# Kernel tuning notes

Measured on AMD Instinct MI355X. Metric: run time of the kernel, lower is better.

The kernel has to match this reference:

```python
import jax, jax.numpy as jnp
import numpy as np

MASK_SUB = 1000000.0  # the module subtracts 1e6 from masked scores (not -inf)

def setup_inputs() -> dict:
    key = jax.random.key(0)
    kq, kk, kv = jax.random.split(key, 3)
    B, S, D = 16, 2048, 64
    q = jax.random.normal(kq, (B, S, D), dtype=jnp.float32)
    k = jax.random.normal(kk, (B, S, D), dtype=jnp.float32)
    v = jax.random.normal(kv, (B, S, D), dtype=jnp.float32)
    return {"q": q, "k": k, "v": v}

def reference(q, k, v):
    d_k = k.shape[-1]
    s = k.shape[-2]
    # scores: [b, s_q, s_k]
    scores = jnp.einsum('bqd,bkd->bqk', q, k) / jnp.sqrt(jnp.asarray(d_k, q.dtype))
    # causal mask: strictly-upper-triangular entries get 1e6 subtracted (matches torch.triu diagonal=1)
    causal = jnp.triu(jnp.ones((s, s), dtype=bool), k=1)
    scores = jnp.where(causal[None, :, :], scores - MASK_SUB, scores)
    weights = jax.nn.softmax(scores, axis=-1)
    return jnp.einsum('bqk,bkd->bqd', weights, v)
```

## Files before the change

### kernel.cpp

```cpp
#include <hip/hip_runtime.h>
#include <stdint.h>


typedef __bf16 bf16x8 __attribute__((ext_vector_type(8)));
typedef float f32x4 __attribute__((ext_vector_type(4)));
typedef float f32x16 __attribute__((ext_vector_type(16)));
typedef uint32_t u32x4 __attribute__((ext_vector_type(4)));

#define NB 16
#define SL 2048
#define DH 64

__device__ __forceinline__ __bf16 f2bf(float f) {
    uint32_t u = __builtin_bit_cast(uint32_t, f);
    u += 0x7FFFu + ((u >> 16) & 1u);
    uint16_t h = (uint16_t)(u >> 16);
    return __builtin_bit_cast(__bf16, h);
}

__device__ __forceinline__ float bf2f(uint16_t u) {
    return __builtin_bit_cast(float, (uint32_t)u << 16);
}

__device__ __forceinline__ uint32_t cvtpk(float lo, float hi) {
    uint32_t r;
    asm("v_cvt_pk_bf16_f32 %0, %1, %2" : "=v"(r) : "v"(lo), "v"(hi));
    return r;
}

__device__ __forceinline__ void load_lds16(const void* g, void* l) {
    __builtin_amdgcn_global_load_lds(
        (const __attribute__((address_space(1))) uint32_t*)g,
        (__attribute__((address_space(3))) uint32_t*)l, 16, 0, 0);
}

__global__ __launch_bounds__(256) void prepass(
        const float* __restrict__ K, const float* __restrict__ V,
        __bf16* __restrict__ Kb, __bf16* __restrict__ Vt) {
    __shared__ float tl[64][68];
    const int b    = blockIdx.x >> 5;
    const int tile = blockIdx.x & 31;
    const int s0   = tile << 6;
    const int t    = threadIdx.x;
    const int r    = t >> 2;
    const int c0   = (t & 3) * 16;

    const float* Kp = K + ((size_t)(b * SL + s0) + r) * DH + c0;
    float4 f0 = ((const float4*)Kp)[0], f1 = ((const float4*)Kp)[1];
    float4 f2 = ((const float4*)Kp)[2], f3 = ((const float4*)Kp)[3];
    bf16x8 w0, w1;
    w0[0]=f2bf(f0.x); w0[1]=f2bf(f0.y); w0[2]=f2bf(f0.z); w0[3]=f2bf(f0.w);
    w0[4]=f2bf(f1.x); w0[5]=f2bf(f1.y); w0[6]=f2bf(f1.z); w0[7]=f2bf(f1.w);
    w1[0]=f2bf(f2.x); w1[1]=f2bf(f2.y); w1[2]=f2bf(f2.z); w1[3]=f2bf(f2.w);
    w1[4]=f2bf(f3.x); w1[5]=f2bf(f3.y); w1[6]=f2bf(f3.z); w1[7]=f2bf(f3.w);
    __bf16* Kbp = Kb + ((size_t)(b * SL + s0) + r) * DH;
    const int j0 = c0 >> 3;
    *(bf16x8*)(Kbp + ((j0       ^ (r & 7)) * 8)) = w0;
    *(bf16x8*)(Kbp + (((j0 + 1) ^ (r & 7)) * 8)) = w1;

    const float* Vp = V + ((size_t)(b * SL + s0) + r) * DH + c0;
    ((float4*)&tl[r][c0])[0] = ((const float4*)Vp)[0];
    ((float4*)&tl[r][c0])[1] = ((const float4*)Vp)[1];
    ((float4*)&tl[r][c0])[2] = ((const float4*)Vp)[2];
    ((float4*)&tl[r][c0])[3] = ((const float4*)Vp)[3];
    __syncthreads();

    __bf16* img = Vt + ((size_t)(b * 32 + tile)) * 4096;
#pragma unroll
    for (int half = 0; half < 2; ++half) {
        const int c = half * 256 + t;
        const int d = c >> 3, slot = c & 7;
        const int jj = slot ^ (d & 7);
        bf16x8 w;
#pragma unroll
        for (int e = 0; e < 8; ++e) w[e] = f2bf(tl[jj * 8 + e][d]);
        *(bf16x8*)(img + c * 8) = w;
    }
}

__global__ __launch_bounds__(256, 3) void attn_fwd(
        const float* __restrict__ Q, const __bf16* __restrict__ Kb,
        const __bf16* __restrict__ Vt, __bf16* __restrict__ part,
        float* __restrict__ lpart, float* __restrict__ O) {
    __shared__ __align__(16) __bf16 lK[3][4096];
    __shared__ __align__(16) __bf16 lV[3][4096];
    __shared__ float lsw[128];

    const int bid = blockIdx.x;
    const int b   = bid & 15;
    const int j   = 39 - (bid >> 4);
    int qb, c;
    if (j < 4)        { qb = j;                 c = 0; }
    else if (j < 12)  { qb = 4 + ((j - 4) >> 1);  c = (j - 4) & 1; }
    else if (j < 24)  { int k = j - 12; qb = 8 + k / 3;    c = k % 3; }
    else              { int k = j - 24; qb = 12 + (k >> 2); c = k & 3; }
    const int nt  = 2 * qb + 2;
    const int nch = (2 * qb + 9) >> 3;
    const int kt0 = c * 8;
    const int kt1 = min(kt0 + 8, nt);

    const int tid  = threadIdx.x;
    const int wave = tid >> 6, lane = tid & 63;
    const int h    = lane >> 5, l32 = lane & 31, x8 = lane & 7;
    const int qg   = qb * 128 + wave * 32 + l32;
    const int dt   = 2 * qb + (wave >> 1);

    const float QSC = 0.125f * 1.44269504088896340736f;
    bf16x8 qf[4];
    const float* qp = Q + ((size_t)b * SL + qg) * DH + h * 8;
#pragma unroll
    for (int s4 = 0; s4 < 4; ++s4) {
        float4 a0 = ((const float4*)(qp + s4 * 16))[0];
        float4 a1 = ((const float4*)(qp + s4 * 16))[1];
        qf[s4][0] = f2bf(a0.x * QSC); qf[s4][1] = f2bf(a0.y * QSC);
        qf[s4][2] = f2bf(a0.z * QSC); qf[s4][3] = f2bf(a0.w * QSC);
        qf[s4][4] = f2bf(a1.x * QSC); qf[s4][5] = f2bf(a1.y * QSC);
        qf[s4][6] = f2bf(a1.z * QSC); qf[s4][7] = f2bf(a1.w * QSC);
    }

    f32x16 acc0 = (f32x16)0.0f, acc1 = (f32x16)0.0f;
    float lsa0 = 0.f, lsa1 = 0.f, lsa2 = 0.f, lsa3 = 0.f;

    const __bf16* Kbase = Kb + (size_t)b * SL * DH;
    const __bf16* Vbase = Vt + (size_t)b * 32 * 4096;

    auto stage = [&](int ti, int bufi) {
        const __bf16* Ks = Kbase + (size_t)ti * 4096;
        const __bf16* Vs = Vbase + (size_t)ti * 4096;
#pragma unroll
        for (int i2 = 0; i2 < 2; ++i2) {
            load_lds16(Ks + (size_t)(i2 * 256 + tid) * 8,
                       &lK[bufi][(i2 * 256 + wave * 64) * 8]);
            load_lds16(Vs + (size_t)(i2 * 256 + tid) * 8,
                       &lV[bufi][(i2 * 256 + wave * 64) * 8]);
        }
    };

    __builtin_amdgcn_sched_barrier(0);
    stage(kt0, kt0 % 3);
    stage(min(kt0 + 1, 31), (kt0 + 1) % 3);
    stage(min(kt0 + 2, 31), (kt0 + 2) % 3);

    for (int kt = kt0; kt < kt1; ++kt) {
        asm volatile("s_waitcnt vmcnt(8)" ::: "memory");
        asm volatile("s_barrier" ::: "memory");
        const __bf16* K_ = lK[kt % 3];
        const __bf16* V_ = lV[kt % 3];

        const bool skip = (wave < 2) && (kt == nt - 1);
        if (!skip) {
            f32x16 sc0 = (f32x16)0.0f, sc1 = (f32x16)0.0f;
            __builtin_amdgcn_s_setprio(1);
#pragma unroll
            for (int s4 = 0; s4 < 4; ++s4) {
                bf16x8 kf0 = *(const bf16x8*)&K_[(l32)      * 64 + (((s4 * 2 + h) ^ x8) << 3)];
                bf16x8 kf1 = *(const bf16x8*)&K_[(32 + l32) * 64 + (((s4 * 2 + h) ^ x8) << 3)];
                sc0 = __builtin_amdgcn_mfma_f32_32x32x16_bf16(kf0, qf[s4], sc0, 0, 0, 0);
                sc1 = __builtin_amdgcn_mfma_f32_32x32x16_bf16(kf1, qf[s4], sc1, 0, 0, 0);
            }
            __builtin_amdgcn_s_setprio(0);

            if (kt >= dt) {
                const int kb = kt * 64;
#pragma unroll
                for (int r = 0; r < 16; ++r) {
                    const int krow = (r & 3) + 8 * (r >> 2) + 4 * h;
                    if (kb + krow > qg)      sc0[r] = -1.0e30f;
                    if (kb + 32 + krow > qg) sc1[r] = -1.0e30f;
                }
            }

#pragma unroll
            for (int r = 0; r < 16; ++r) {
                sc0[r] = __builtin_amdgcn_exp2f(sc0[r]);
                sc1[r] = __builtin_amdgcn_exp2f(sc1[r]);
            }
#pragma unroll
            for (int r = 0; r < 16; r += 4) {
                lsa0 += sc0[r + 0] + sc1[r + 0];
                lsa1 += sc0[r + 1] + sc1[r + 1];
                lsa2 += sc0[r + 2] + sc1[r + 2];
                lsa3 += sc0[r + 3] + sc1[r + 3];
            }

            bf16x8 af[4];
#pragma unroll
            for (int ks = 0; ks < 4; ++ks) {
                const int jj = (ks & 1) * 8;
                const f32x16& sg = (ks & 2) ? sc1 : sc0;
                uint32_t u0 = cvtpk(sg[jj + 0], sg[jj + 1]);
                uint32_t u1 = cvtpk(sg[jj + 2], sg[jj + 3]);
                uint32_t u2 = cvtpk(sg[jj + 4], sg[jj + 5]);
                uint32_t u3 = cvtpk(sg[jj + 6], sg[jj + 7]);
                auto r0 = __builtin_amdgcn_permlane32_swap(u0, u2, false, false);
                auto r1 = __builtin_amdgcn_permlane32_swap(u1, u3, false, false);
                u32x4 w; w[0] = r0[0]; w[1] = r1[0]; w[2] = r0[1]; w[3] = r1[1];
                af[ks] = __builtin_bit_cast(bf16x8, w);
            }

            __builtin_amdgcn_s_setprio(1);
#pragma unroll
            for (int ks = 0; ks < 4; ++ks) {
                bf16x8 vf0 = *(const bf16x8*)&V_[(l32)      * 64 + ((((ks << 1) + h) ^ x8) << 3)];
                bf16x8 vf1 = *(const bf16x8*)&V_[(32 + l32) * 64 + ((((ks << 1) + h) ^ x8) << 3)];
                acc0 = __builtin_amdgcn_mfma_f32_32x32x16_bf16(af[ks], vf0, acc0, 0, 0, 0);
                acc1 = __builtin_amdgcn_mfma_f32_32x32x16_bf16(af[ks], vf1, acc1, 0, 0, 0);
            }
            __builtin_amdgcn_s_setprio(0);
        }

        asm volatile("s_barrier" ::: "memory");
        stage(min(kt + 3, 31), kt % 3);
    }

    asm volatile("s_waitcnt vmcnt(0)" ::: "memory");

    float ls = (lsa0 + lsa1) + (lsa2 + lsa3);
    ls += __shfl_xor(ls, 32);
    if (h == 0) lsw[wave * 32 + l32] = ls;
    __syncthreads();

    if (nch == 1) {
        float* Ob = O + ((size_t)(b * SL + qb * 128 + wave * 32)) * DH;
#pragma unroll
        for (int r = 0; r < 16; ++r) {
            const int crow = (r & 3) + 8 * (r >> 2) + 4 * h;
            const float inv = 1.0f / lsw[wave * 32 + crow];
            Ob[(size_t)crow * DH + l32]      = acc0[r] * inv;
            Ob[(size_t)crow * DH + l32 + 32] = acc1[r] * inv;
        }
        return;
    }

#pragma unroll
    for (int r = 0; r < 16; ++r) {
        const int qrow = qb * 128 + wave * 32 + (r & 3) + 8 * (r >> 2) + 4 * h;
        __bf16* pp = part + ((size_t)(b * SL + qrow) * 4 + c) * DH + l32;
        pp[0]  = f2bf(acc0[r]);
        pp[32] = f2bf(acc1[r]);
    }
    if (h == 0)
        lpart[(size_t)(b * SL + qg) * 4 + c] = ls;
}

__global__ __launch_bounds__(256) void combine(
        const __bf16* __restrict__ part, const float* __restrict__ lpart,
        float* __restrict__ O) {
    const int tid = threadIdx.x;
    const int bpb = 96;
    const int b   = blockIdx.x / bpb;
    const int ri  = blockIdx.x % bpb;
    const int lrow = 512 + ri * 16 + (tid >> 4);
    const size_t r = (size_t)b * SL + lrow;
    const int d4  = tid & 15;
    const int qb  = lrow >> 7;
    const int nch = (2 * qb + 9) >> 3;
    float4 s = make_float4(0.f, 0.f, 0.f, 0.f);
    float ls = 0.f;
    for (int c = 0; c < nch; ++c) {
        ushort4 u = *(const ushort4*)(part + (r * 4 + c) * DH + d4 * 4);
        s.x += bf2f(u.x); s.y += bf2f(u.y); s.z += bf2f(u.z); s.w += bf2f(u.w);
        ls += lpart[r * 4 + c];
    }
    const float inv = 1.0f / ls;
    float4 o; o.x = s.x * inv; o.y = s.y * inv; o.z = s.z * inv; o.w = s.w * inv;
    *(float4*)(O + r * DH + d4 * 4) = o;
}

extern "C" void kernel_launch(void* const* d_in, const int* in_sizes, int n_in,
                              void* d_out, int out_size, void* d_ws, size_t ws_size,
                              hipStream_t stream) {
    const float* q = (const float*)d_in[0];
    const float* k = (const float*)d_in[1];
    const float* v = (const float*)d_in[2];
    float* o = (float*)d_out;
    __bf16* Kb   = (__bf16*)d_ws;
    __bf16* Vt   = Kb + (size_t)NB * SL * DH;
    __bf16* pt   = (__bf16*)((char*)d_ws + (8u << 20));
    float*  lp   = (float*)((char*)d_ws + (24u << 20));
    hipLaunchKernelGGL(prepass, dim3(NB * 32), dim3(256), 0, stream, k, v, Kb, Vt);
    hipLaunchKernelGGL(attn_fwd, dim3(640), dim3(256), 0, stream, q, Kb, Vt, pt, lp, o);
    hipLaunchKernelGGL(combine, dim3(NB * 96), dim3(256), 0, stream, pt, lp, o);
}
```

Before: 96.43 us.

## Split key tile across wave pairs with 64-row query tiles and LDS reduction

Query tiles shrink from 128 to 64 rows and the grid doubles to 1280 blocks. Each pair of waves now splits the 64 keys of a tile into two 32-key halves, and the two halves' partial outputs and row sums are reduced through LDS at the end. The LDS ring drops from triple to double buffering and occupancy is raised to 4 blocks per CU. The aim is better load balance and more parallelism for causal attention. In exchange it adds an LDS reduction, extra syncs, and a shallower prefetch depth, and each K/V tile is now staged by more blocks.

Measured after the change: 99.48 us. 1.03x slower.

```diff
diff --git a/kernel.cpp b/kernel.cpp
--- a/kernel.cpp
+++ b/kernel.cpp
@@ -78,32 +78,33 @@
     }
 }
 
-__global__ __launch_bounds__(256, 3) void attn_fwd(
+__global__ __launch_bounds__(256, 4) void attn_fwd(
         const float* __restrict__ Q, const __bf16* __restrict__ Kb,
         const __bf16* __restrict__ Vt, __bf16* __restrict__ part,
         float* __restrict__ lpart, float* __restrict__ O) {
-    __shared__ __align__(16) __bf16 lK[3][4096];
-    __shared__ __align__(16) __bf16 lV[3][4096];
-    __shared__ float lsw[128];
+    __shared__ __align__(16) __bf16 lK[2][4096];
+    __shared__ __align__(16) __bf16 lV[2][4096];
+    __shared__ float lsP[64];
+    __shared__ float lsw[64];
 
     const int bid = blockIdx.x;
     const int b   = bid & 15;
-    const int j   = 39 - (bid >> 4);
-    int qb, c;
-    if (j < 4)        { qb = j;                 c = 0; }
-    else if (j < 12)  { qb = 4 + ((j - 4) >> 1);  c = (j - 4) & 1; }
-    else if (j < 24)  { int k = j - 12; qb = 8 + k / 3;    c = k % 3; }
-    else              { int k = j - 24; qb = 12 + (k >> 2); c = k & 3; }
-    const int nt  = 2 * qb + 2;
-    const int nch = (2 * qb + 9) >> 3;
+    const int j   = bid >> 4;
+    int qt, c;
+    if (j < 32)       { qt = 31 - (j >> 2);              c = j & 3; }
+    else if (j < 56)  { int k = j - 32; qt = 23 - k / 3;   c = k % 3; }
+    else if (j < 72)  { int k = j - 56; qt = 15 - (k >> 1); c = k & 1; }
+    else              { qt = 79 - j;                     c = 0; }
+    const int nt  = qt + 1;
+    const int nch = (qt >> 3) + 1;
     const int kt0 = c * 8;
     const int kt1 = min(kt0 + 8, nt);
 
     const int tid  = threadIdx.x;
     const int wave = tid >> 6, lane = tid & 63;
+    const int pair = wave >> 1, half = wave & 1;
     const int h    = lane >> 5, l32 = lane & 31, x8 = lane & 7;
-    const int qg   = qb * 128 + wave * 32 + l32;
-    const int dt   = 2 * qb + (wave >> 1);
+    const int qg   = qt * 64 + pair * 32 + l32;
 
     const float QSC = 0.125f * 1.44269504088896340736f;
     bf16x8 qf[4];
@@ -124,7 +125,8 @@
     const __bf16* Kbase = Kb + (size_t)b * SL * DH;
     const __bf16* Vbase = Vt + (size_t)b * 32 * 4096;
 
-    auto stage = [&](int ti, int bufi) {
+    auto stage = [&](int ti) {
+        const int bufi = ti & 1;
         const __bf16* Ks = Kbase + (size_t)ti * 4096;
         const __bf16* Vs = Vbase + (size_t)ti * 4096;
 #pragma unroll
@@ -137,95 +139,111 @@
     };
 
     __builtin_amdgcn_sched_barrier(0);
-    stage(kt0, kt0 % 3);
-    stage(min(kt0 + 1, 31), (kt0 + 1) % 3);
-    stage(min(kt0 + 2, 31), (kt0 + 2) % 3);
+    stage(kt0);
+    stage(min(kt0 + 1, 31));
 
     for (int kt = kt0; kt < kt1; ++kt) {
-        asm volatile("s_waitcnt vmcnt(8)" ::: "memory");
+        if (kt + 1 < kt1) asm volatile("s_waitcnt vmcnt(4)" ::: "memory");
+        else              asm volatile("s_waitcnt vmcnt(0)" ::: "memory");
         asm volatile("s_barrier" ::: "memory");
-        const __bf16* K_ = lK[kt % 3];
-        const __bf16* V_ = lV[kt % 3];
-
-        const bool skip = (wave < 2) && (kt == nt - 1);
+        const __bf16* K_ = lK[kt & 1];
+        const __bf16* V_ = lV[kt & 1];
+
+        const bool skip = (wave == 1) && (kt == qt);
         if (!skip) {
-            f32x16 sc0 = (f32x16)0.0f, sc1 = (f32x16)0.0f;
+            f32x16 sc = (f32x16)0.0f;
             __builtin_amdgcn_s_setprio(1);
 #pragma unroll
             for (int s4 = 0; s4 < 4; ++s4) {
-                bf16x8 kf0 = *(const bf16x8*)&K_[(l32)      * 64 + (((s4 * 2 + h) ^ x8) << 3)];
-                bf16x8 kf1 = *(const bf16x8*)&K_[(32 + l32) * 64 + (((s4 * 2 + h) ^ x8) << 3)];
-                sc0 = __builtin_amdgcn_mfma_f32_32x32x16_bf16(kf0, qf[s4], sc0, 0, 0, 0);
-                sc1 = __builtin_amdgcn_mfma_f32_32x32x16_bf16(kf1, qf[s4], sc1, 0, 0, 0);
+                bf16x8 kf = *(const bf16x8*)&K_[(half * 32 + l32) * 64 + (((s4 * 2 + h) ^ x8) << 3)];
+                sc = __builtin_amdgcn_mfma_f32_32x32x16_bf16(kf, qf[s4], sc, 0, 0, 0);
             }
             __builtin_amdgcn_s_setprio(0);
 
-            if (kt >= dt) {
-                const int kb = kt * 64;
+            if (kt == qt) {
+                const int kb = kt * 64 + half * 32;
 #pragma unroll
                 for (int r = 0; r < 16; ++r) {
-                    const int krow = (r & 3) + 8 * (r >> 2) + 4 * h;
-                    if (kb + krow > qg)      sc0[r] = -1.0e30f;
-                    if (kb + 32 + krow > qg) sc1[r] = -1.0e30f;
+                    const int key = kb + (r & 3) + 8 * (r >> 2) + 4 * h;
+                    if (key > qg) sc[r] = -1.0e30f;
                 }
             }
 
 #pragma unroll
-            for (int r = 0; r < 16; ++r) {
-                sc0[r] = __builtin_amdgcn_exp2f(sc0[r]);
-                sc1[r] = __builtin_amdgcn_exp2f(sc1[r]);
-            }
+            for (int r = 0; r < 16; ++r) sc[r] = __builtin_amdgcn_exp2f(sc[r]);
 #pragma unroll
             for (int r = 0; r < 16; r += 4) {
-                lsa0 += sc0[r + 0] + sc1[r + 0];
-                lsa1 += sc0[r + 1] + sc1[r + 1];
-                lsa2 += sc0[r + 2] + sc1[r + 2];
-                lsa3 += sc0[r + 3] + sc1[r + 3];
-            }
-
-            bf16x8 af[4];
-#pragma unroll
-            for (int ks = 0; ks < 4; ++ks) {
-                const int jj = (ks & 1) * 8;
-                const f32x16& sg = (ks & 2) ? sc1 : sc0;
-                uint32_t u0 = cvtpk(sg[jj + 0], sg[jj + 1]);
-                uint32_t u1 = cvtpk(sg[jj + 2], sg[jj + 3]);
-                uint32_t u2 = cvtpk(sg[jj + 4], sg[jj + 5]);
-                uint32_t u3 = cvtpk(sg[jj + 6], sg[jj + 7]);
+                lsa0 += sc[r + 0]; lsa1 += sc[r + 1];
+                lsa2 += sc[r + 2]; lsa3 += sc[r + 3];
+            }
+
+            bf16x8 af[2];
+#pragma unroll
+            for (int kk = 0; kk < 2; ++kk) {
+                const int jj = kk * 8;
+                uint32_t u0 = cvtpk(sc[jj + 0], sc[jj + 1]);
+                uint32_t u1 = cvtpk(sc[jj + 2], sc[jj + 3]);
+                uint32_t u2 = cvtpk(sc[jj + 4], sc[jj + 5]);
+                uint32_t u3 = cvtpk(sc[jj + 6], sc[jj + 7]);
                 auto r0 = __builtin_amdgcn_permlane32_swap(u0, u2, false, false);
                 auto r1 = __builtin_amdgcn_permlane32_swap(u1, u3, false, false);
                 u32x4 w; w[0] = r0[0]; w[1] = r1[0]; w[2] = r0[1]; w[3] = r1[1];
-                af[ks] = __builtin_bit_cast(bf16x8, w);
+                af[kk] = __builtin_bit_cast(bf16x8, w);
             }
 
             __builtin_amdgcn_s_setprio(1);
 #pragma unroll
-            for (int ks = 0; ks < 4; ++ks) {
-                bf16x8 vf0 = *(const bf16x8*)&V_[(l32)      * 64 + ((((ks << 1) + h) ^ x8) << 3)];
-                bf16x8 vf1 = *(const bf16x8*)&V_[(32 + l32) * 64 + ((((ks << 1) + h) ^ x8) << 3)];
-                acc0 = __builtin_amdgcn_mfma_f32_32x32x16_bf16(af[ks], vf0, acc0, 0, 0, 0);
-                acc1 = __builtin_amdgcn_mfma_f32_32x32x16_bf16(af[ks], vf1, acc1, 0, 0, 0);
+            for (int kk = 0; kk < 2; ++kk) {
+                const int ksg = half * 2 + kk;
+                bf16x8 vf0 = *(const bf16x8*)&V_[(l32)      * 64 + ((((ksg << 1) + h) ^ x8) << 3)];
+                bf16x8 vf1 = *(const bf16x8*)&V_[(32 + l32) * 64 + ((((ksg << 1) + h) ^ x8) << 3)];
+                acc0 = __builtin_amdgcn_mfma_f32_32x32x16_bf16(af[kk], vf0, acc0, 0, 0, 0);
+                acc1 = __builtin_amdgcn_mfma_f32_32x32x16_bf16(af[kk], vf1, acc1, 0, 0, 0);
             }
             __builtin_amdgcn_s_setprio(0);
         }
 
         asm volatile("s_barrier" ::: "memory");
-        stage(min(kt + 3, 31), kt % 3);
+        stage(min(kt + 2, 31));
     }
 
     asm volatile("s_waitcnt vmcnt(0)" ::: "memory");
+    __syncthreads();
 
     float ls = (lsa0 + lsa1) + (lsa2 + lsa3);
     ls += __shfl_xor(ls, 32);
-    if (h == 0) lsw[wave * 32 + l32] = ls;
-    __syncthreads();
-
-    if (nch == 1) {
-        float* Ob = O + ((size_t)(b * SL + qb * 128 + wave * 32)) * DH;
+
+    float* M = (float*)lK;
+    if (half == 1) {
 #pragma unroll
         for (int r = 0; r < 16; ++r) {
             const int crow = (r & 3) + 8 * (r >> 2) + 4 * h;
-            const float inv = 1.0f / lsw[wave * 32 + crow];
+            M[(pair * 32 + crow) * 64 + l32]      = acc0[r];
+            M[(pair * 32 + crow) * 64 + 32 + l32] = acc1[r];
+        }
+        if (h == 0) lsP[pair * 32 + l32] = ls;
+    }
+    __syncthreads();
+    if (half == 0) {
+#pragma unroll
+        for (int r = 0; r < 16; ++r) {
+            const int crow = (r & 3) + 8 * (r >> 2) + 4 * h;
+            acc0[r] += M[(pair * 32 + crow) * 64 + l32];
+            acc1[r] += M[(pair * 32 + crow) * 64 + 32 + l32];
+        }
+        ls += lsP[pair * 32 + l32];
+        if (h == 0) lsw[pair * 32 + l32] = ls;
+    }
+    __syncthreads();
+
+    if (half != 0) return;
+
+    if (nch == 1) {
+        float* Ob = O + ((size_t)(b * SL + qt * 64 + pair * 32)) * DH;
+#pragma unroll
+        for (int r = 0; r < 16; ++r) {
+            const int crow = (r & 3) + 8 * (r >> 2) + 4 * h;
+            const float inv = 1.0f / lsw[pair * 32 + crow];
             Ob[(size_t)crow * DH + l32]      = acc0[r] * inv;
             Ob[(size_t)crow * DH + l32 + 32] = acc1[r] * inv;
         }
@@ -234,7 +252,7 @@
 
 #pragma unroll
     for (int r = 0; r < 16; ++r) {
-        const int qrow = qb * 128 + wave * 32 + (r & 3) + 8 * (r >> 2) + 4 * h;
+        const int qrow = qt * 64 + pair * 32 + (r & 3) + 8 * (r >> 2) + 4 * h;
         __bf16* pp = part + ((size_t)(b * SL + qrow) * 4 + c) * DH + l32;
         pp[0]  = f2bf(acc0[r]);
         pp[32] = f2bf(acc1[r]);
@@ -253,8 +271,8 @@
     const int lrow = 512 + ri * 16 + (tid >> 4);
     const size_t r = (size_t)b * SL + lrow;
     const int d4  = tid & 15;
-    const int qb  = lrow >> 7;
-    const int nch = (2 * qb + 9) >> 3;
+    const int qt  = lrow >> 6;
+    const int nch = (qt >> 3) + 1;
     float4 s = make_float4(0.f, 0.f, 0.f, 0.f);
     float ls = 0.f;
     for (int c = 0; c < nch; ++c) {
@@ -279,6 +297,6 @@
     __bf16* pt   = (__bf16*)((char*)d_ws + (8u << 20));
     float*  lp   = (float*)((char*)d_ws + (24u << 20));
     hipLaunchKernelGGL(prepass, dim3(NB * 32), dim3(256), 0, stream, k, v, Kb, Vt);
-    hipLaunchKernelGGL(attn_fwd, dim3(640), dim3(256), 0, stream, q, Kb, Vt, pt, lp, o);
+    hipLaunchKernelGGL(attn_fwd, dim3(1280), dim3(256), 0, stream, q, Kb, Vt, pt, lp, o);
     hipLaunchKernelGGL(combine, dim3(NB * 96), dim3(256), 0, stream, pt, lp, o);
 }
```
